# Kernel optimization log

Measured on AMD Instinct MI355X. Metric: run time of the kernel, lower is better.

Reference implementation:

```python
import jax, jax.numpy as jnp
import numpy as np

N_STATIONS = 100000
N_TIME = 365
N_NEIGHBORS = 5
SMOOTHING = 0.1


def setup_inputs() -> dict:
    key = jax.random.key(0)
    k = jax.random.split(key, 6)
    N, T, K = N_STATIONS, N_TIME, N_NEIGHBORS
    time_vector = jnp.arange(T, dtype=jnp.float32) / 365.25  # years
    constant_offset = jax.random.normal(k[0], (N,), jnp.float32) * 10.0
    linear_trend = jax.random.normal(k[1], (N,), jnp.float32) * 5.0  # mm/yr (ps00_rates buffer)
    seasonal_amplitudes = jax.random.uniform(k[2], (N, 4), jnp.float32) * 6.0
    seasonal_phases = jax.random.uniform(k[3], (N, 4), jnp.float32) * (2.0 * np.pi)
    neighbor_indices = jax.random.randint(k[4], (N, K), 0, N)
    w = jax.random.uniform(k[5], (N, K), jnp.float32) + 1e-3
    neighbor_weights = w / jnp.sum(w, axis=1, keepdims=True)  # row-normalized, like exp-dist weights
    periods = jnp.array([0.25, 0.5, 1.0, 2.0], dtype=jnp.float32)
    return {
        'time_vector': time_vector,
        'constant_offset': constant_offset,
        'linear_trend': linear_trend,
        'seasonal_amplitudes': seasonal_amplitudes,
        'seasonal_phases': seasonal_phases,
        'neighbor_weights': neighbor_weights,
        'periods': periods,
        'neighbor_indices': neighbor_indices,
    }


def _smooth(p, neighbor_indices, neighbor_weights):
    # p: [N, 4]; vectorized version of per-station loop: gather + weighted mean
    nb = p[neighbor_indices]                                   # [N, K, 4]
    avg = jnp.einsum('nkf,nk->nf', nb, neighbor_weights)       # [N, 4]
    return (1.0 - SMOOTHING) * p + SMOOTHING * avg


def reference(time_vector, constant_offset, linear_trend, seasonal_amplitudes,
              seasonal_phases, neighbor_weights, periods, neighbor_indices):
    amps = _smooth(seasonal_amplitudes, neighbor_indices, neighbor_weights)   # [N, 4]
    phs = _smooth(seasonal_phases, neighbor_indices, neighbor_weights)        # [N, 4]
    t = time_vector[None, :]                                                  # [1, T]
    signals = constant_offset[:, None] + linear_trend[:, None] * t           # [N, T]
    two_pi = jnp.float32(2.0 * np.pi)
    for f in range(4):  # fixed small set of seasonal periods
        freq = 1.0 / periods[f]
        signals = signals + amps[:, f:f + 1] * jnp.sin(two_pi * freq * t + phs[:, f:f + 1])
    return signals
```

## Files before the change

### kernel.cpp

```cpp
#include <hip/hip_runtime.h>
#include <math.h>

typedef float f32x2 __attribute__((ext_vector_type(2)));
typedef float f32x4 __attribute__((ext_vector_type(4)));

#define TWO_PI 6.283185307179586f
#define SMOOTH 0.1f
#define SPW 4
#define WAVES 4
#define BLOCK 256
#define SPB (SPW * WAVES)
#define NPAIR 3

__device__ __forceinline__ f32x2 sp2(float x) { f32x2 r; r.x = x; r.y = x; return r; }
__device__ __forceinline__ float rlane(float v, int l) {
    return __uint_as_float((unsigned)__builtin_amdgcn_readlane((int)__float_as_uint(v), l));
}
__device__ __forceinline__ void wait_lgkm() {
    asm volatile("s_waitcnt lgkmcnt(0)" ::: "memory");
}

template<int TT>
__global__ __launch_bounds__(BLOCK, 4) void fused_v18(
    const float* __restrict__ time_vector,
    const float* __restrict__ constant_offset,
    const float* __restrict__ linear_trend,
    const float* __restrict__ amps,
    const float* __restrict__ phs,
    const float* __restrict__ wgt,
    const float* __restrict__ periods,
    const int*   __restrict__ nbidx,
    float* __restrict__ out,
    int N, int T_rt, int K)
{
    const int T = (TT > 0) ? TT : T_rt;
    extern __shared__ float slab[];

    const int tid    = threadIdx.x;
    const int wave   = tid >> 6;
    const int lane   = tid & 63;
    const int wbase  = blockIdx.x * SPB + wave * SPW;

    if (wbase >= N) return;
    int send = N - wbase; if (send > SPW) send = SPW;

    int sid = wbase + (lane & (SPW - 1));
    if (sid >= N) sid = N - 1;

    float4 a = reinterpret_cast<const float4*>(amps)[sid];
    float4 p = reinterpret_cast<const float4*>(phs)[sid];

    int   nb[5]; float w[5];
    __builtin_memcpy(nb, nbidx + (size_t)sid * K, 5 * sizeof(int));
    __builtin_memcpy(w,  wgt   + (size_t)sid * K, 5 * sizeof(float));

    float av0 = 0.f, av1 = 0.f, av2 = 0.f, av3 = 0.f;
    float pv0 = 0.f, pv1 = 0.f, pv2 = 0.f, pv3 = 0.f;
    #pragma unroll
    for (int k = 0; k < 5; ++k) {
        float4 na = reinterpret_cast<const float4*>(amps)[nb[k]];
        float4 np = reinterpret_cast<const float4*>(phs)[nb[k]];
        av0 += w[k] * na.x; av1 += w[k] * na.y; av2 += w[k] * na.z; av3 += w[k] * na.w;
        pv0 += w[k] * np.x; pv1 += w[k] * np.y; pv2 += w[k] * np.z; pv3 += w[k] * np.w;
    }
    float sa0 = (1.0f - SMOOTH) * a.x + SMOOTH * av0;
    float sa1 = (1.0f - SMOOTH) * a.y + SMOOTH * av1;
    float sa2 = (1.0f - SMOOTH) * a.z + SMOOTH * av2;
    float sa3 = (1.0f - SMOOTH) * a.w + SMOOTH * av3;
    float sp0 = (1.0f - SMOOTH) * p.x + SMOOTH * pv0;
    float sp1 = (1.0f - SMOOTH) * p.y + SMOOTH * pv1;
    float sp2v = (1.0f - SMOOTH) * p.z + SMOOTH * pv2;
    float sp3 = (1.0f - SMOOTH) * p.w + SMOOTH * pv3;

    float cc = constant_offset[sid];
    float cm = linear_trend[sid];
    float cA0 = sa0 * __cosf(sp0),  cB0 = sa0 * __sinf(sp0);
    float cA1 = sa1 * __cosf(sp1),  cB1 = sa1 * __sinf(sp1);
    float cA2 = sa2 * __cosf(sp2v), cB2 = sa2 * __sinf(sp2v);
    float cA3 = sa3 * __cosf(sp3),  cB3 = sa3 * __sinf(sp3);

    const float w0 = TWO_PI / periods[0];
    const float w1 = TWO_PI / periods[1];
    const float w2 = TWO_PI / periods[2];
    const float w3 = TWO_PI / periods[3];

    f32x2 tv[NPAIR];
    f32x2 bs[NPAIR][4], bc[NPAIR][4];
    bool full[NPAIR], any[NPAIR];
    const int t0 = 2 * lane;

    #pragma unroll
    for (int q = 0; q < NPAIR; ++q) {
        const int t = t0 + 128 * q;
        const bool v0 = (t < T), v1 = (t + 1 < T);
        any[q] = v0; full[q] = v1;
        float ta = v0 ? time_vector[t]     : 0.f;
        float tb = v1 ? time_vector[t + 1] : 0.f;
        f32x2 tvp; tvp.x = ta; tvp.y = tb;
        tv[q] = tvp;
        #pragma unroll
        for (int f = 0; f < 4; ++f) {
            const float wf = (f == 0) ? w0 : (f == 1) ? w1 : (f == 2) ? w2 : w3;
            f32x2 s, c;
            s.x = __sinf(wf * ta); s.y = __sinf(wf * tb);
            c.x = __cosf(wf * ta); c.y = __cosf(wf * tb);
            bs[q][f] = s; bc[q][f] = c;
        }
    }

    float* wrows = slab + (size_t)(wave * SPW) * T;

    if (send == SPW) {
        #pragma unroll
        for (int j = 0; j < SPW; ++j) {
            float sc  = rlane(cc,  j), sm  = rlane(cm,  j);
            float sA0 = rlane(cA0, j), sB0 = rlane(cB0, j);
            float sA1 = rlane(cA1, j), sB1 = rlane(cB1, j);
            float sA2 = rlane(cA2, j), sB2 = rlane(cB2, j);
            float sA3 = rlane(cA3, j), sB3 = rlane(cB3, j);
            float* lrow = wrows + j * T;

            #pragma unroll
            for (int q = 0; q < NPAIR; ++q) {
                f32x2 sig = sp2(sc) + sp2(sm) * tv[q];
                sig += sp2(sA0) * bs[q][0] + sp2(sB0) * bc[q][0];
                sig += sp2(sA1) * bs[q][1] + sp2(sB1) * bc[q][1];
                sig += sp2(sA2) * bs[q][2] + sp2(sB2) * bc[q][2];
                sig += sp2(sA3) * bs[q][3] + sp2(sB3) * bc[q][3];
                const int t = t0 + 128 * q;
                if (full[q]) { lrow[t] = sig.x; lrow[t + 1] = sig.y; }
                else if (any[q]) { lrow[t] = sig.x; }
            }
        }

        wait_lgkm();

        const f32x4* lsrc = reinterpret_cast<const f32x4*>(wrows);
        f32x4* gdst = reinterpret_cast<f32x4*>(out + (size_t)wbase * T);

        if (TT == 365) {
            f32x4 v0_ = lsrc[lane];         f32x4 v1_ = lsrc[lane + 64];
            f32x4 v2_ = lsrc[lane + 128];   f32x4 v3_ = lsrc[lane + 192];
            f32x4 v4_ = lsrc[lane + 256];
            const bool extra = (lane < 45);
            f32x4 v5_;
            if (extra) v5_ = lsrc[lane + 320];

            __builtin_nontemporal_store(v0_, gdst + lane);
            __builtin_nontemporal_store(v1_, gdst + lane + 64);
            __builtin_nontemporal_store(v2_, gdst + lane + 128);
            __builtin_nontemporal_store(v3_, gdst + lane + 192);
            __builtin_nontemporal_store(v4_, gdst + lane + 256);
            if (extra) __builtin_nontemporal_store(v5_, gdst + lane + 320);
        } else {
            const int nch = (SPW * T) >> 2;
            for (int i = lane; i < nch; i += 64) {
                f32x4 v = lsrc[i];
                __builtin_nontemporal_store(v, gdst + i);
            }
        }
    } else {
        float* obase = out + (size_t)wbase * T;
        for (int j = 0; j < send; ++j) {
            float sc  = rlane(cc,  j), sm  = rlane(cm,  j);
            float sA0 = rlane(cA0, j), sB0 = rlane(cB0, j);
            float sA1 = rlane(cA1, j), sB1 = rlane(cB1, j);
            float sA2 = rlane(cA2, j), sB2 = rlane(cB2, j);
            float sA3 = rlane(cA3, j), sB3 = rlane(cB3, j);
            float* orow = obase + (size_t)j * T;
            #pragma unroll
            for (int q = 0; q < NPAIR; ++q) {
                f32x2 sig = sp2(sc) + sp2(sm) * tv[q];
                sig += sp2(sA0) * bs[q][0] + sp2(sB0) * bc[q][0];
                sig += sp2(sA1) * bs[q][1] + sp2(sB1) * bc[q][1];
                sig += sp2(sA2) * bs[q][2] + sp2(sB2) * bc[q][2];
                sig += sp2(sA3) * bs[q][3] + sp2(sB3) * bc[q][3];
                const int t = t0 + 128 * q;
                if (full[q]) { orow[t] = sig.x; orow[t + 1] = sig.y; }
                else if (any[q]) { orow[t] = sig.x; }
            }
        }
    }
}

extern "C" void kernel_launch(void* const* d_in, const int* in_sizes, int n_in,
                              void* d_out, int out_size, void* d_ws, size_t ws_size,
                              hipStream_t stream)
{
    const float* time_vector     = (const float*)d_in[0];
    const float* constant_offset = (const float*)d_in[1];
    const float* linear_trend    = (const float*)d_in[2];
    const float* amps            = (const float*)d_in[3];
    const float* phs             = (const float*)d_in[4];
    const float* wgt             = (const float*)d_in[5];
    const float* periods         = (const float*)d_in[6];
    const int*   nbidx           = (const int*)d_in[7];

    int T = in_sizes[0];
    int N = in_sizes[1];
    int K = in_sizes[5] / N;
    float* out = (float*)d_out;

    int grid = (N + SPB - 1) / SPB;
    size_t shmem = (size_t)SPB * T * sizeof(float);
    if (T == 365) {
        fused_v18<365><<<grid, BLOCK, shmem, stream>>>(
            time_vector, constant_offset, linear_trend, amps, phs, wgt,
            periods, nbidx, out, N, T, K);
    } else {
        fused_v18<0><<<grid, BLOCK, shmem, stream>>>(
            time_vector, constant_offset, linear_trend, amps, phs, wgt,
            periods, nbidx, out, N, T, K);
    }
}
```

Measured before the change: 43.68 us.

## Raise stations per wave to 16, derive harmonics by double-angle, restructure LDS store

Each wave now handles 16 stations instead of 4, using 2 waves of 128 threads per block. The per-lane time basis, with its sin/cos evaluations, is therefore reused across four times as many stations. When the periods form a doubling chain, the lower-period sin/cos values are derived from the longest period with double-angle identities rather than separate transcendental calls. The copy from shared memory to global memory is rewritten for the larger 16x365 slab. In exchange, shared memory per block grows, launch bounds are relaxed, the identity chain adds some rounding error, and the grid has fewer, larger blocks.

```diff
diff --git a/kernel.cpp b/kernel.cpp
--- a/kernel.cpp
+++ b/kernel.cpp
@@ -6,9 +6,9 @@
 
 #define TWO_PI 6.283185307179586f
 #define SMOOTH 0.1f
-#define SPW 4
-#define WAVES 4
-#define BLOCK 256
+#define SPW 16
+#define WAVES 2
+#define BLOCK 128
 #define SPB (SPW * WAVES)
 #define NPAIR 3
 
@@ -21,7 +21,7 @@
 }
 
 template<int TT>
-__global__ __launch_bounds__(BLOCK, 4) void fused_v18(
+__global__ __launch_bounds__(BLOCK) void fused_v19(
     const float* __restrict__ time_vector,
     const float* __restrict__ constant_offset,
     const float* __restrict__ linear_trend,
@@ -79,10 +79,14 @@
     float cA2 = sa2 * __cosf(sp2v), cB2 = sa2 * __sinf(sp2v);
     float cA3 = sa3 * __cosf(sp3),  cB3 = sa3 * __sinf(sp3);
 
-    const float w0 = TWO_PI / periods[0];
-    const float w1 = TWO_PI / periods[1];
-    const float w2 = TWO_PI / periods[2];
-    const float w3 = TWO_PI / periods[3];
+    const float P0 = periods[0], P1 = periods[1], P2 = periods[2], P3 = periods[3];
+    const float w0 = TWO_PI / P0;
+    const float w1 = TWO_PI / P1;
+    const float w2 = TWO_PI / P2;
+    const float w3 = TWO_PI / P3;
+    const bool pow2chain = (fabsf(P3 - 2.f * P2) < 1e-6f * P3) &&
+                           (fabsf(P2 - 2.f * P1) < 1e-6f * P2) &&
+                           (fabsf(P1 - 2.f * P0) < 1e-6f * P1);
 
     f32x2 tv[NPAIR];
     f32x2 bs[NPAIR][4], bc[NPAIR][4];
@@ -98,13 +102,29 @@
         float tb = v1 ? time_vector[t + 1] : 0.f;
         f32x2 tvp; tvp.x = ta; tvp.y = tb;
         tv[q] = tvp;
-        #pragma unroll
-        for (int f = 0; f < 4; ++f) {
-            const float wf = (f == 0) ? w0 : (f == 1) ? w1 : (f == 2) ? w2 : w3;
-            f32x2 s, c;
-            s.x = __sinf(wf * ta); s.y = __sinf(wf * tb);
-            c.x = __cosf(wf * ta); c.y = __cosf(wf * tb);
-            bs[q][f] = s; bc[q][f] = c;
+
+        if (pow2chain) {
+            float s3a = __sinf(w3 * ta), c3a = __cosf(w3 * ta);
+            float s3b = __sinf(w3 * tb), c3b = __cosf(w3 * tb);
+            float s2a = 2.f * s3a * c3a, c2a = 1.f - 2.f * s3a * s3a;
+            float s2b = 2.f * s3b * c3b, c2b = 1.f - 2.f * s3b * s3b;
+            float s1a = 2.f * s2a * c2a, c1a = 1.f - 2.f * s2a * s2a;
+            float s1b = 2.f * s2b * c2b, c1b = 1.f - 2.f * s2b * s2b;
+            float s0a = 2.f * s1a * c1a, c0a = 1.f - 2.f * s1a * s1a;
+            float s0b = 2.f * s1b * c1b, c0b = 1.f - 2.f * s1b * s1b;
+            bs[q][0].x = s0a; bs[q][0].y = s0b; bc[q][0].x = c0a; bc[q][0].y = c0b;
+            bs[q][1].x = s1a; bs[q][1].y = s1b; bc[q][1].x = c1a; bc[q][1].y = c1b;
+            bs[q][2].x = s2a; bs[q][2].y = s2b; bc[q][2].x = c2a; bc[q][2].y = c2b;
+            bs[q][3].x = s3a; bs[q][3].y = s3b; bc[q][3].x = c3a; bc[q][3].y = c3b;
+        } else {
+            #pragma unroll
+            for (int f = 0; f < 4; ++f) {
+                const float wf = (f == 0) ? w0 : (f == 1) ? w1 : (f == 2) ? w2 : w3;
+                f32x2 s, c;
+                s.x = __sinf(wf * ta); s.y = __sinf(wf * tb);
+                c.x = __cosf(wf * ta); c.y = __cosf(wf * tb);
+                bs[q][f] = s; bc[q][f] = c;
+            }
         }
     }
 
@@ -139,19 +159,32 @@
         f32x4* gdst = reinterpret_cast<f32x4*>(out + (size_t)wbase * T);
 
         if (TT == 365) {
-            f32x4 v0_ = lsrc[lane];         f32x4 v1_ = lsrc[lane + 64];
-            f32x4 v2_ = lsrc[lane + 128];   f32x4 v3_ = lsrc[lane + 192];
-            f32x4 v4_ = lsrc[lane + 256];
-            const bool extra = (lane < 45);
-            f32x4 v5_;
-            if (extra) v5_ = lsrc[lane + 320];
-
-            __builtin_nontemporal_store(v0_, gdst + lane);
-            __builtin_nontemporal_store(v1_, gdst + lane + 64);
-            __builtin_nontemporal_store(v2_, gdst + lane + 128);
-            __builtin_nontemporal_store(v3_, gdst + lane + 192);
-            __builtin_nontemporal_store(v4_, gdst + lane + 256);
-            if (extra) __builtin_nontemporal_store(v5_, gdst + lane + 320);
+            #pragma unroll
+            for (int half = 0; half < 2; ++half) {
+                const int base = half * 704;
+                f32x4 v0_ = lsrc[base + lane];        f32x4 v1_ = lsrc[base + lane + 64];
+                f32x4 v2_ = lsrc[base + lane + 128];  f32x4 v3_ = lsrc[base + lane + 192];
+                f32x4 v4_ = lsrc[base + lane + 256];  f32x4 v5_ = lsrc[base + lane + 320];
+                f32x4 v6_ = lsrc[base + lane + 384];  f32x4 v7_ = lsrc[base + lane + 448];
+                f32x4 v8_ = lsrc[base + lane + 512];  f32x4 v9_ = lsrc[base + lane + 576];
+                f32x4 va_ = lsrc[base + lane + 640];
+
+                __builtin_nontemporal_store(v0_, gdst + base + lane);
+                __builtin_nontemporal_store(v1_, gdst + base + lane + 64);
+                __builtin_nontemporal_store(v2_, gdst + base + lane + 128);
+                __builtin_nontemporal_store(v3_, gdst + base + lane + 192);
+                __builtin_nontemporal_store(v4_, gdst + base + lane + 256);
+                __builtin_nontemporal_store(v5_, gdst + base + lane + 320);
+                __builtin_nontemporal_store(v6_, gdst + base + lane + 384);
+                __builtin_nontemporal_store(v7_, gdst + base + lane + 448);
+                __builtin_nontemporal_store(v8_, gdst + base + lane + 512);
+                __builtin_nontemporal_store(v9_, gdst + base + lane + 576);
+                __builtin_nontemporal_store(va_, gdst + base + lane + 640);
+            }
+            if (lane < 52) {
+                f32x4 vr_ = lsrc[1408 + lane];
+                __builtin_nontemporal_store(vr_, gdst + 1408 + lane);
+            }
         } else {
             const int nch = (SPW * T) >> 2;
             for (int i = lane; i < nch; i += 64) {
@@ -204,11 +237,11 @@
     int grid = (N + SPB - 1) / SPB;
     size_t shmem = (size_t)SPB * T * sizeof(float);
     if (T == 365) {
-        fused_v18<365><<<grid, BLOCK, shmem, stream>>>(
+        fused_v19<365><<<grid, BLOCK, shmem, stream>>>(
             time_vector, constant_offset, linear_trend, amps, phs, wgt,
             periods, nbidx, out, N, T, K);
     } else {
-        fused_v18<0><<<grid, BLOCK, shmem, stream>>>(
+        fused_v19<0><<<grid, BLOCK, shmem, stream>>>(
             time_vector, constant_offset, linear_trend, amps, phs, wgt,
             periods, nbidx, out, N, T, K);
     }
```

Measured after the change: 44.83 us. 1.03x slower.
